# Kernel tuning notes

Hardware: AMD Instinct MI355X
Metric: run time of the kernel (lower is better)

The kernel has to match this reference:

```python
import jax, jax.numpy as jnp
import numpy as np

B, N, F_DIM = 32, 1024, 128
ALPHA = 0.2        # LeakyReLU negative slope
PAD = -9e15        # pad_sequence padding value in the original
DENSITY = 0.05


def setup_inputs() -> dict:
    key = jax.random.key(0)
    k1, k2, k3 = jax.random.split(key, 3)
    # sparse 0/1 adjacency with self-loops so every node has degree >= 1
    adj = (jax.random.uniform(k1, (B, N, N)) < DENSITY).astype(jnp.float32)
    eye = jnp.eye(N, dtype=jnp.float32)[None, :, :]
    adj = jnp.maximum(adj, eye)
    feats = jax.random.normal(k2, (B, N, F_DIM), dtype=jnp.float32)
    # xavier_uniform with leaky_relu gain on a [2F, 1]
    gain = float(np.sqrt(2.0 / (1.0 + ALPHA ** 2)))
    bound = gain * float(np.sqrt(6.0 / (2 * F_DIM + 1)))
    a = jax.random.uniform(k3, (2 * F_DIM, 1), minval=-bound, maxval=bound,
                           dtype=jnp.float32)
    return {"batch_graphs": adj, "batch_features": feats, "a": a}


def reference(batch_graphs, batch_features, a):
    # e_ij = LeakyReLU([h_i || h_j] @ a) decomposes as (h_i @ a1) + (h_j @ a2)
    s_src = batch_features @ a[:F_DIM, 0]   # [B, N] contribution of node i
    s_dst = batch_features @ a[F_DIM:, 0]   # [B, N] contribution of neighbor j
    e = s_src[:, :, None] + s_dst[:, None, :]            # [B, N, N]
    e = jnp.where(e >= 0, e, ALPHA * e)                   # LeakyReLU
    mask = batch_graphs == 1
    e = jnp.where(mask, e, PAD)                           # pad non-edges like pad_sequence
    att = jax.nn.softmax(e, axis=-1)                      # segmented softmax over neighbors
    att = jnp.where(mask, att, 0.0)                       # scatter back only real edges
    return att
```

## Files before the change

### kernel.cpp

```cpp
#include <hip/hip_runtime.h>
#include <hip/hip_bf16.h>
#include <stdint.h>

#define B_DIM 32
#define N_DIM 1024
#define F_DIM 128
#define ALPHA 0.2f
#define NROWS (B_DIM * N_DIM)
#define TAIL_ROWS 128
#define SCORE_BYTES ((size_t)(2 * NROWS) * sizeof(float))

__device__ __forceinline__ bool probe_is_f32(const void* adj) {
    return *(const uint32_t*)adj == 0x3F800000u;
}

template <bool F32>
__device__ __forceinline__ float* score_base(float* ws, int use_ws, void* out) {
    if (use_ws) return ws;
    const size_t out_bytes = (size_t)NROWS * N_DIM * (F32 ? 4 : 2);
    return (float*)((char*)out + out_bytes - SCORE_BYTES);
}

template <bool F32>
__device__ __forceinline__ void scores_body(
    const void* __restrict__ feats_v, const void* __restrict__ a_v,
    float* ws, int use_ws, void* out)
{
    float* base  = score_base<F32>(ws, use_ws, out);
    float* s_src = base;
    float* s_dst = base + NROWS;

    const int wid  = threadIdx.x >> 6;
    const int lane = threadIdx.x & 63;
    const int row  = blockIdx.x * 4 + wid;
    const int f0   = lane * 2;

    float x0, x1, a10, a11, a20, a21;
    if (F32) {
        const float* fp = (const float*)feats_v + (size_t)row * F_DIM + f0;
        const float* ap = (const float*)a_v;
        x0 = fp[0]; x1 = fp[1];
        a10 = ap[f0];         a11 = ap[f0 + 1];
        a20 = ap[F_DIM + f0]; a21 = ap[F_DIM + f0 + 1];
    } else {
        const __hip_bfloat16* fp = (const __hip_bfloat16*)feats_v + (size_t)row * F_DIM + f0;
        const __hip_bfloat16* ap = (const __hip_bfloat16*)a_v;
        x0  = __bfloat162float(fp[0]);           x1  = __bfloat162float(fp[1]);
        a10 = __bfloat162float(ap[f0]);          a11 = __bfloat162float(ap[f0 + 1]);
        a20 = __bfloat162float(ap[F_DIM + f0]);  a21 = __bfloat162float(ap[F_DIM + f0 + 1]);
    }

    float v1 = x0 * a10 + x1 * a11;
    float v2 = x0 * a20 + x1 * a21;
    #pragma unroll
    for (int off = 32; off > 0; off >>= 1) {
        v1 += __shfl_down(v1, off, 64);
        v2 += __shfl_down(v2, off, 64);
    }
    if (lane == 0) { s_src[row] = v1; s_dst[row] = v2; }
}

__global__ __launch_bounds__(256) void scores_kernel(
    const void* __restrict__ adj, const void* __restrict__ feats,
    const void* __restrict__ a, float* ws, int use_ws, void* out)
{
    if (probe_is_f32(adj)) scores_body<true>(feats, a, ws, use_ws, out);
    else                   scores_body<false>(feats, a, ws, use_ws, out);
}

template <bool F32>
__device__ __forceinline__ void softmax_core(
    const void* __restrict__ adj_v, void* __restrict__ out_v,
    int row, float ssrc, const float* sdst, float* wmax, float* wsum)
{
    const int tid  = threadIdx.x;
    const int lane = tid & 63;
    const int wid  = tid >> 6;

    bool valid[4];
    if (F32) {
        const uint4 av = ((const uint4*)((const float*)adj_v + (size_t)row * N_DIM))[tid];
        valid[0] = av.x != 0u; valid[1] = av.y != 0u;
        valid[2] = av.z != 0u; valid[3] = av.w != 0u;
    } else {
        const ushort4 av = ((const ushort4*)((const __hip_bfloat16*)adj_v + (size_t)row * N_DIM))[tid];
        valid[0] = av.x != 0; valid[1] = av.y != 0;
        valid[2] = av.z != 0; valid[3] = av.w != 0;
    }

    const int j0 = tid * 4;
    float e[4];
    float lmax = -1e30f;
    #pragma unroll
    for (int k = 0; k < 4; ++k) {
        float t = ssrc + sdst[j0 + k];
        t = (t >= 0.0f) ? t : ALPHA * t;
        e[k] = t;
        if (valid[k]) lmax = fmaxf(lmax, t);
    }

    #pragma unroll
    for (int off = 32; off > 0; off >>= 1)
        lmax = fmaxf(lmax, __shfl_down(lmax, off, 64));
    if (lane == 0) wmax[wid] = lmax;
    __syncthreads();
    const float m = fmaxf(fmaxf(wmax[0], wmax[1]), fmaxf(wmax[2], wmax[3]));

    float p[4], lsum = 0.0f;
    #pragma unroll
    for (int k = 0; k < 4; ++k) {
        p[k] = valid[k] ? __expf(e[k] - m) : 0.0f;
        lsum += p[k];
    }
    #pragma unroll
    for (int off = 32; off > 0; off >>= 1)
        lsum += __shfl_down(lsum, off, 64);
    if (lane == 0) wsum[wid] = lsum;
    __syncthreads();
    const float inv = 1.0f / (wsum[0] + wsum[1] + wsum[2] + wsum[3]);

    if (F32) {
        float4 o = make_float4(p[0] * inv, p[1] * inv, p[2] * inv, p[3] * inv);
        ((float4*)((float*)out_v + (size_t)row * N_DIM))[tid] = o;
    } else {
        union { ushort4 u4; __hip_bfloat16 h[4]; } o;
        #pragma unroll
        for (int k = 0; k < 4; ++k) o.h[k] = __float2bfloat16(p[k] * inv);
        ((ushort4*)((__hip_bfloat16*)out_v + (size_t)row * N_DIM))[tid] = o.u4;
    }
}

template <bool F32>
__device__ __forceinline__ void main_body(
    const void* __restrict__ adj_v, float* ws, int use_ws, void* out_v)
{
    const int row = blockIdx.x;
    const int b   = row >> 10;
    const int tid = threadIdx.x;

    float* base  = score_base<F32>(ws, use_ws, out_v);
    const float* s_src = base;
    const float* s_dst = base + NROWS + (size_t)b * N_DIM;

    __shared__ float sdst[N_DIM];
    __shared__ float wmax[4];
    __shared__ float wsum[4];

    #pragma unroll
    for (int k = 0; k < 4; ++k)
        sdst[tid + 256 * k] = s_dst[tid + 256 * k];
    const float ssrc = s_src[row];
    __syncthreads();

    softmax_core<F32>(adj_v, out_v, row, ssrc, sdst, wmax, wsum);
}

__global__ __launch_bounds__(256) void main_kernel(
    const void* __restrict__ adj, float* ws, int use_ws, void* out)
{
    if (probe_is_f32(adj)) main_body<true>(adj, ws, use_ws, out);
    else                   main_body<false>(adj, ws, use_ws, out);
}

template <bool F32>
__device__ __forceinline__ void tail_body(
    const void* __restrict__ adj_v, const void* __restrict__ feats_v,
    const void* __restrict__ a_v, void* __restrict__ out_v)
{
    const int row = NROWS - TAIL_ROWS + blockIdx.x;
    const int b   = row >> 10;
    const int tid = threadIdx.x;

    __shared__ float sdst[N_DIM];
    __shared__ float ssrc_sh;
    __shared__ float wmax[4];
    __shared__ float wsum[4];

    #pragma unroll
    for (int k = 0; k < 4; ++k) {
        const int j = tid * 4 + k;
        float acc = 0.0f;
        if (F32) {
            const float* fp = (const float*)feats_v + ((size_t)b * N_DIM + j) * F_DIM;
            const float* ap = (const float*)a_v + F_DIM;
            #pragma unroll 8
            for (int f = 0; f < F_DIM; ++f) acc += fp[f] * ap[f];
        } else {
            const __hip_bfloat16* fp = (const __hip_bfloat16*)feats_v + ((size_t)b * N_DIM + j) * F_DIM;
            const __hip_bfloat16* ap = (const __hip_bfloat16*)a_v + F_DIM;
            #pragma unroll 8
            for (int f = 0; f < F_DIM; ++f)
                acc += __bfloat162float(fp[f]) * __bfloat162float(ap[f]);
        }
        sdst[j] = acc;
    }

    if (tid < 64) {
        const int f0 = tid * 2;
        float x0, x1, a0, a1;
        if (F32) {
            const float* fp = (const float*)feats_v + (size_t)row * F_DIM + f0;
            const float* ap = (const float*)a_v;
            x0 = fp[0]; x1 = fp[1]; a0 = ap[f0]; a1 = ap[f0 + 1];
        } else {
            const __hip_bfloat16* fp = (const __hip_bfloat16*)feats_v + (size_t)row * F_DIM + f0;
            const __hip_bfloat16* ap = (const __hip_bfloat16*)a_v;
            x0 = __bfloat162float(fp[0]); x1 = __bfloat162float(fp[1]);
            a0 = __bfloat162float(ap[f0]); a1 = __bfloat162float(ap[f0 + 1]);
        }
        float v = x0 * a0 + x1 * a1;
        #pragma unroll
        for (int off = 32; off > 0; off >>= 1)
            v += __shfl_down(v, off, 64);
        if (tid == 0) ssrc_sh = v;
    }
    __syncthreads();

    softmax_core<F32>(adj_v, out_v, row, ssrc_sh, sdst, wmax, wsum);
}

__global__ __launch_bounds__(256) void tail_kernel(
    const void* __restrict__ adj, const void* __restrict__ feats,
    const void* __restrict__ a, void* __restrict__ out)
{
    if (probe_is_f32(adj)) tail_body<true>(adj, feats, a, out);
    else                   tail_body<false>(adj, feats, a, out);
}

extern "C" void kernel_launch(void* const* d_in, const int* in_sizes, int n_in,
                              void* d_out, int out_size, void* d_ws, size_t ws_size,
                              hipStream_t stream) {
    const void* adj   = d_in[0];
    const void* feats = d_in[1];
    const void* a     = d_in[2];

    const int use_ws = (ws_size >= SCORE_BYTES) ? 1 : 0;
    float* ws = (float*)d_ws;

    scores_kernel<<<NROWS / 4, 256, 0, stream>>>(adj, feats, a, ws, use_ws, d_out);
    main_kernel<<<NROWS - TAIL_ROWS, 256, 0, stream>>>(adj, ws, use_ws, d_out);
    tail_kernel<<<TAIL_ROWS, 256, 0, stream>>>(adj, feats, a, d_out);
}
```

Measured before the change: 263.0 us.

## Compute softmax rows per wavefront and collapse the tail into one block

The main kernel now gives each 64-lane wavefront a full row. It uses xor-shuffle reductions, reads s_dst straight from global memory, and drops the shared-memory staging and block barriers. Output goes through nontemporal vector stores. The tail kernel no longer recomputes scores from the features: one 1024-thread block stages the last batch's scores in LDS before overwriting the output region that holds them. Scores are now always kept in the tail of the output buffer rather than the workspace, and running the tail on a single block serialises 128 rows on one CU.

```diff
diff --git a/kernel.cpp b/kernel.cpp
--- a/kernel.cpp
+++ b/kernel.cpp
@@ -8,25 +8,34 @@
 #define ALPHA 0.2f
 #define NROWS (B_DIM * N_DIM)
 #define TAIL_ROWS 128
+#define MAIN_ROWS (NROWS - TAIL_ROWS)
 #define SCORE_BYTES ((size_t)(2 * NROWS) * sizeof(float))
+
+typedef float          vf4 __attribute__((ext_vector_type(4)));
+typedef unsigned short vh4 __attribute__((ext_vector_type(4)));
+typedef unsigned int   vu4 __attribute__((ext_vector_type(4)));
+
+__device__ __forceinline__ unsigned short f32_to_bf16_bits(float f) {
+    union { __hip_bfloat16 h; unsigned short u; } cvt;
+    cvt.h = __float2bfloat16(f);
+    return cvt.u;
+}
 
 __device__ __forceinline__ bool probe_is_f32(const void* adj) {
     return *(const uint32_t*)adj == 0x3F800000u;
 }
 
 template <bool F32>
-__device__ __forceinline__ float* score_base(float* ws, int use_ws, void* out) {
-    if (use_ws) return ws;
+__device__ __forceinline__ float* score_base(void* out) {
     const size_t out_bytes = (size_t)NROWS * N_DIM * (F32 ? 4 : 2);
     return (float*)((char*)out + out_bytes - SCORE_BYTES);
 }
 
 template <bool F32>
 __device__ __forceinline__ void scores_body(
-    const void* __restrict__ feats_v, const void* __restrict__ a_v,
-    float* ws, int use_ws, void* out)
-{
-    float* base  = score_base<F32>(ws, use_ws, out);
+    const void* __restrict__ feats_v, const void* __restrict__ a_v, void* out)
+{
+    float* base  = score_base<F32>(out);
     float* s_src = base;
     float* s_dst = base + NROWS;
 
@@ -62,169 +71,129 @@
 
 __global__ __launch_bounds__(256) void scores_kernel(
     const void* __restrict__ adj, const void* __restrict__ feats,
-    const void* __restrict__ a, float* ws, int use_ws, void* out)
-{
-    if (probe_is_f32(adj)) scores_body<true>(feats, a, ws, use_ws, out);
-    else                   scores_body<false>(feats, a, ws, use_ws, out);
-}
-
-template <bool F32>
-__device__ __forceinline__ void softmax_core(
+    const void* __restrict__ a, void* out)
+{
+    if (probe_is_f32(adj)) scores_body<true>(feats, a, out);
+    else                   scores_body<false>(feats, a, out);
+}
+
+template <bool F32>
+__device__ __forceinline__ void wave_softmax_row(
     const void* __restrict__ adj_v, void* __restrict__ out_v,
-    int row, float ssrc, const float* sdst, float* wmax, float* wsum)
-{
+    int row, float ssrc, const float* __restrict__ sdst )
+{
+    const int lane = threadIdx.x & 63;
+
+    float p[16];
+    uint32_t vmask = 0;
+    float lmax = -1e30f;
+
+    #pragma unroll
+    for (int c = 0; c < 4; ++c) {
+        const int idx = c * 64 + lane;
+        const vf4 sd = ((const vf4*)sdst)[idx];
+        bool v[4];
+        if (F32) {
+            const vu4 av = ((const vu4*)((const float*)adj_v + (size_t)row * N_DIM))[idx];
+            v[0] = av.x != 0u; v[1] = av.y != 0u; v[2] = av.z != 0u; v[3] = av.w != 0u;
+        } else {
+            const vh4 av = ((const vh4*)((const __hip_bfloat16*)adj_v + (size_t)row * N_DIM))[idx];
+            v[0] = av.x != 0; v[1] = av.y != 0; v[2] = av.z != 0; v[3] = av.w != 0;
+        }
+        const float sdk[4] = {sd.x, sd.y, sd.z, sd.w};
+        #pragma unroll
+        for (int k = 0; k < 4; ++k) {
+            float t = ssrc + sdk[k];
+            t = (t >= 0.0f) ? t : ALPHA * t;
+            p[c * 4 + k] = t;
+            if (v[k]) { lmax = fmaxf(lmax, t); vmask |= 1u << (c * 4 + k); }
+        }
+    }
+
+    #pragma unroll
+    for (int off = 1; off < 64; off <<= 1)
+        lmax = fmaxf(lmax, __shfl_xor(lmax, off, 64));
+
+    float lsum = 0.0f;
+    #pragma unroll
+    for (int i = 0; i < 16; ++i) {
+        p[i] = (vmask >> i) & 1 ? __expf(p[i] - lmax) : 0.0f;
+        lsum += p[i];
+    }
+    #pragma unroll
+    for (int off = 1; off < 64; off <<= 1)
+        lsum += __shfl_xor(lsum, off, 64);
+    const float inv = 1.0f / lsum;
+
+    #pragma unroll
+    for (int c = 0; c < 4; ++c) {
+        const int idx = c * 64 + lane;
+        if (F32) {
+            vf4 o;
+            o.x = p[c*4+0] * inv; o.y = p[c*4+1] * inv;
+            o.z = p[c*4+2] * inv; o.w = p[c*4+3] * inv;
+            __builtin_nontemporal_store(o,
+                ((vf4*)((float*)out_v + (size_t)row * N_DIM)) + idx);
+        } else {
+            vh4 o;
+            o.x = f32_to_bf16_bits(p[c*4+0] * inv);
+            o.y = f32_to_bf16_bits(p[c*4+1] * inv);
+            o.z = f32_to_bf16_bits(p[c*4+2] * inv);
+            o.w = f32_to_bf16_bits(p[c*4+3] * inv);
+            __builtin_nontemporal_store(o,
+                ((vh4*)((__hip_bfloat16*)out_v + (size_t)row * N_DIM)) + idx);
+        }
+    }
+}
+
+template <bool F32>
+__device__ __forceinline__ void main_body(const void* __restrict__ adj_v, void* out_v)
+{
+    const int wid = threadIdx.x >> 6;
+    const int row = blockIdx.x * 4 + wid;
+    const int b   = row >> 10;
+
+    const float* base = score_base<F32>(out_v);
+    const float  ssrc = base[row];
+    const float* sdst = base + NROWS + (size_t)b * N_DIM;
+
+    wave_softmax_row<F32>(adj_v, out_v, row, ssrc, sdst);
+}
+
+__global__ __launch_bounds__(256) void main_kernel(
+    const void* __restrict__ adj, void* out)
+{
+    if (probe_is_f32(adj)) main_body<true>(adj, out);
+    else                   main_body<false>(adj, out);
+}
+
+template <bool F32>
+__device__ __forceinline__ void tail_body(const void* __restrict__ adj_v, void* out_v)
+{
+    __shared__ float sdst_sh[N_DIM];
+    __shared__ float ssrc_sh[TAIL_ROWS];
+
     const int tid  = threadIdx.x;
-    const int lane = tid & 63;
-    const int wid  = tid >> 6;
-
-    bool valid[4];
-    if (F32) {
-        const uint4 av = ((const uint4*)((const float*)adj_v + (size_t)row * N_DIM))[tid];
-        valid[0] = av.x != 0u; valid[1] = av.y != 0u;
-        valid[2] = av.z != 0u; valid[3] = av.w != 0u;
-    } else {
-        const ushort4 av = ((const ushort4*)((const __hip_bfloat16*)adj_v + (size_t)row * N_DIM))[tid];
-        valid[0] = av.x != 0; valid[1] = av.y != 0;
-        valid[2] = av.z != 0; valid[3] = av.w != 0;
-    }
-
-    const int j0 = tid * 4;
-    float e[4];
-    float lmax = -1e30f;
-    #pragma unroll
-    for (int k = 0; k < 4; ++k) {
-        float t = ssrc + sdst[j0 + k];
-        t = (t >= 0.0f) ? t : ALPHA * t;
-        e[k] = t;
-        if (valid[k]) lmax = fmaxf(lmax, t);
-    }
-
-    #pragma unroll
-    for (int off = 32; off > 0; off >>= 1)
-        lmax = fmaxf(lmax, __shfl_down(lmax, off, 64));
-    if (lane == 0) wmax[wid] = lmax;
+    const float* base = score_base<F32>(out_v);
+
+    sdst_sh[tid] = base[NROWS + (B_DIM - 1) * N_DIM + tid];
+    if (tid < TAIL_ROWS) ssrc_sh[tid] = base[MAIN_ROWS + tid];
     __syncthreads();
-    const float m = fmaxf(fmaxf(wmax[0], wmax[1]), fmaxf(wmax[2], wmax[3]));
-
-    float p[4], lsum = 0.0f;
-    #pragma unroll
-    for (int k = 0; k < 4; ++k) {
-        p[k] = valid[k] ? __expf(e[k] - m) : 0.0f;
-        lsum += p[k];
-    }
-    #pragma unroll
-    for (int off = 32; off > 0; off >>= 1)
-        lsum += __shfl_down(lsum, off, 64);
-    if (lane == 0) wsum[wid] = lsum;
-    __syncthreads();
-    const float inv = 1.0f / (wsum[0] + wsum[1] + wsum[2] + wsum[3]);
-
-    if (F32) {
-        float4 o = make_float4(p[0] * inv, p[1] * inv, p[2] * inv, p[3] * inv);
-        ((float4*)((float*)out_v + (size_t)row * N_DIM))[tid] = o;
-    } else {
-        union { ushort4 u4; __hip_bfloat16 h[4]; } o;
-        #pragma unroll
-        for (int k = 0; k < 4; ++k) o.h[k] = __float2bfloat16(p[k] * inv);
-        ((ushort4*)((__hip_bfloat16*)out_v + (size_t)row * N_DIM))[tid] = o.u4;
-    }
-}
-
-template <bool F32>
-__device__ __forceinline__ void main_body(
-    const void* __restrict__ adj_v, float* ws, int use_ws, void* out_v)
-{
-    const int row = blockIdx.x;
-    const int b   = row >> 10;
-    const int tid = threadIdx.x;
-
-    float* base  = score_base<F32>(ws, use_ws, out_v);
-    const float* s_src = base;
-    const float* s_dst = base + NROWS + (size_t)b * N_DIM;
-
-    __shared__ float sdst[N_DIM];
-    __shared__ float wmax[4];
-    __shared__ float wsum[4];
-
-    #pragma unroll
-    for (int k = 0; k < 4; ++k)
-        sdst[tid + 256 * k] = s_dst[tid + 256 * k];
-    const float ssrc = s_src[row];
-    __syncthreads();
-
-    softmax_core<F32>(adj_v, out_v, row, ssrc, sdst, wmax, wsum);
-}
-
-__global__ __launch_bounds__(256) void main_kernel(
-    const void* __restrict__ adj, float* ws, int use_ws, void* out)
-{
-    if (probe_is_f32(adj)) main_body<true>(adj, ws, use_ws, out);
-    else                   main_body<false>(adj, ws, use_ws, out);
-}
-
-template <bool F32>
-__device__ __forceinline__ void tail_body(
-    const void* __restrict__ adj_v, const void* __restrict__ feats_v,
-    const void* __restrict__ a_v, void* __restrict__ out_v)
-{
-    const int row = NROWS - TAIL_ROWS + blockIdx.x;
-    const int b   = row >> 10;
-    const int tid = threadIdx.x;
-
-    __shared__ float sdst[N_DIM];
-    __shared__ float ssrc_sh;
-    __shared__ float wmax[4];
-    __shared__ float wsum[4];
-
-    #pragma unroll
-    for (int k = 0; k < 4; ++k) {
-        const int j = tid * 4 + k;
-        float acc = 0.0f;
-        if (F32) {
-            const float* fp = (const float*)feats_v + ((size_t)b * N_DIM + j) * F_DIM;
-            const float* ap = (const float*)a_v + F_DIM;
-            #pragma unroll 8
-            for (int f = 0; f < F_DIM; ++f) acc += fp[f] * ap[f];
-        } else {
-            const __hip_bfloat16* fp = (const __hip_bfloat16*)feats_v + ((size_t)b * N_DIM + j) * F_DIM;
-            const __hip_bfloat16* ap = (const __hip_bfloat16*)a_v + F_DIM;
-            #pragma unroll 8
-            for (int f = 0; f < F_DIM; ++f)
-                acc += __bfloat162float(fp[f]) * __bfloat162float(ap[f]);
-        }
-        sdst[j] = acc;
-    }
-
-    if (tid < 64) {
-        const int f0 = tid * 2;
-        float x0, x1, a0, a1;
-        if (F32) {
-            const float* fp = (const float*)feats_v + (size_t)row * F_DIM + f0;
-            const float* ap = (const float*)a_v;
-            x0 = fp[0]; x1 = fp[1]; a0 = ap[f0]; a1 = ap[f0 + 1];
-        } else {
-            const __hip_bfloat16* fp = (const __hip_bfloat16*)feats_v + (size_t)row * F_DIM + f0;
-            const __hip_bfloat16* ap = (const __hip_bfloat16*)a_v;
-            x0 = __bfloat162float(fp[0]); x1 = __bfloat162float(fp[1]);
-            a0 = __bfloat162float(ap[f0]); a1 = __bfloat162float(ap[f0 + 1]);
-        }
-        float v = x0 * a0 + x1 * a1;
-        #pragma unroll
-        for (int off = 32; off > 0; off >>= 1)
-            v += __shfl_down(v, off, 64);
-        if (tid == 0) ssrc_sh = v;
-    }
-    __syncthreads();
-
-    softmax_core<F32>(adj_v, out_v, row, ssrc_sh, sdst, wmax, wsum);
-}
-
-__global__ __launch_bounds__(256) void tail_kernel(
-    const void* __restrict__ adj, const void* __restrict__ feats,
-    const void* __restrict__ a, void* __restrict__ out)
-{
-    if (probe_is_f32(adj)) tail_body<true>(adj, feats, a, out);
-    else                   tail_body<false>(adj, feats, a, out);
+
+    const int wid = tid >> 6;
+    #pragma unroll
+    for (int r = 0; r < TAIL_ROWS / 16; ++r) {
+        const int rr  = wid * (TAIL_ROWS / 16) + r;
+        const int row = MAIN_ROWS + rr;
+        wave_softmax_row<F32>(adj_v, out_v, row, ssrc_sh[rr], sdst_sh);
+    }
+}
+
+__global__ __launch_bounds__(1024) void tail_kernel(
+    const void* __restrict__ adj, void* out)
+{
+    if (probe_is_f32(adj)) tail_body<true>(adj, out);
+    else                   tail_body<false>(adj, out);
 }
 
 extern "C" void kernel_launch(void* const* d_in, const int* in_sizes, int n_in,
@@ -233,11 +202,9 @@
     const void* adj   = d_in[0];
     const void* feats = d_in[1];
     const void* a     = d_in[2];
-
-    const int use_ws = (ws_size >= SCORE_BYTES) ? 1 : 0;
-    float* ws = (float*)d_ws;
-
-    scores_kernel<<<NROWS / 4, 256, 0, stream>>>(adj, feats, a, ws, use_ws, d_out);
-    main_kernel<<<NROWS - TAIL_ROWS, 256, 0, stream>>>(adj, ws, use_ws, d_out);
-    tail_kernel<<<TAIL_ROWS, 256, 0, stream>>>(adj, feats, a, d_out);
-}
+    (void)d_ws; (void)ws_size;
+
+    scores_kernel<<<NROWS / 4, 256, 0, stream>>>(adj, feats, a, d_out);
+    main_kernel<<<MAIN_ROWS / 4, 256, 0, stream>>>(adj, d_out);
+    tail_kernel<<<1, 1024, 0, stream>>>(adj, d_out);
+}
```

After: 266.3 us. No clear change (+1.3%).
